# Kernel optimization log

Hardware: AMD Instinct MI355X
Metric: run time of the kernel (lower is better)

## Reference

```python
import jax, jax.numpy as jnp
import numpy as np

IN_F = 128
OUT_F = 128
GROUPS = 8
NUM_F = 8
B = 16
NP_ = 4096


def setup_inputs() -> dict:
    key = jax.random.key(0)
    ks = jax.random.split(key, 6)
    x = jax.random.normal(ks[0], (B, NP_, IN_F), dtype=jnp.float32)
    grid = jnp.arange(NUM_F, dtype=jnp.float32) + 1.0                      # [num_f]
    base_weight = jax.random.normal(ks[1], (OUT_F, IN_F), dtype=jnp.float32) * 0.05
    scale_sp = jnp.ones((OUT_F,), dtype=jnp.float32)
    coef = jax.random.uniform(ks[2], (GROUPS, 1, NUM_F), dtype=jnp.float32)
    conv_w = jax.random.normal(ks[3], (NUM_F, OUT_F, IN_F), dtype=jnp.float32) * 0.05  # grouped 1x1 conv
    conv_b = jax.random.normal(ks[4], (NUM_F, OUT_F), dtype=jnp.float32) * 0.05
    return {"x": x, "grid": grid, "base_weight": base_weight,
            "scale_sp": scale_sp, "coef": coef, "conv_w": conv_w, "conv_b": conv_b}


def reference(x, grid, base_weight, scale_sp, coef, conv_w, conv_b):
    Bd, Nd, D = x.shape
    num_f = grid.shape[0]
    groups = coef.shape[0]
    gsz = D // groups
    xf = x.reshape(Bd * Nd, D)                                  # [batch, in]
    # base path: SiLU then linear (no bias)
    base = jax.nn.silu(xf) @ base_weight.T                       # [batch, out]
    # spline path: sin(grid * x), broadcast coef per (group, f)
    s = jnp.sin(grid[None, :, None] * xf[:, None, :])            # [batch, num_f, in]
    cm = coef[:, 0, :].T                                         # [num_f, groups]
    s = s.reshape(-1, num_f, groups, gsz) * cm[None, :, :, None]
    s = s.reshape(-1, num_f, D)                                  # [batch, num_f, in]
    # grouped 1x1 conv == per-f GEMM
    spline = jnp.einsum('bfi,foi->bfo', s, conv_w) + conv_b[None]
    spline = spline.sum(axis=1) * scale_sp                       # [batch, out]
    out = (base + spline).reshape(Bd, Nd, -1)
    return out
```

## Files before the change

### kernel.cpp

```cpp
#include <hip/hip_runtime.h>
#include <hip/hip_bf16.h>
#include <stdint.h>

#define IN_F   128
#define OUT_F  128
#define NUM_F  8
#define NROWS  (16*4096)

typedef __bf16  bf16x8  __attribute__((ext_vector_type(8)));
typedef float   f32x16  __attribute__((ext_vector_type(16)));

#define LDS_HALF  (9*8*2*64*16)
#define WP_CHUNKS (2*9*8*2*64)
#define WP_BYTES  (WP_CHUNKS*16)
#define BIAS_OFF  WP_BYTES

__global__ __launch_bounds__(256) void skan_prep(
    const float* __restrict__ base_w,
    const float* __restrict__ scale,
    const float* __restrict__ coef,
    const float* __restrict__ conv_w,
    const float* __restrict__ conv_b,
    __bf16* __restrict__ Wp, float* __restrict__ bias)
{
    int gid = blockIdx.x * 256 + threadIdx.x;
    int flat = gid;
    int l  = flat & 63;  flat >>= 6;
    int t2 = flat & 1;   flat >>= 1;
    int s  = flat & 7;   flat >>= 3;
    int fb = flat % 9;
    int h2 = flat / 9;
    int n  = h2 * 64 + t2 * 32 + (l & 31);
    int k0 = s * 16 + (l >> 5) * 8;
    __bf16* dst = Wp + (size_t)gid * 8;
    if (fb == 0) {
        const float4* b4 = (const float4*)(base_w + n * IN_F + k0);
        float4 a = b4[0], b = b4[1];
        dst[0]=(__bf16)a.x; dst[1]=(__bf16)a.y; dst[2]=(__bf16)a.z; dst[3]=(__bf16)a.w;
        dst[4]=(__bf16)b.x; dst[5]=(__bf16)b.y; dst[6]=(__bf16)b.z; dst[7]=(__bf16)b.w;
    } else {
        int f = fb - 1;
        float sc = scale[n];
        const float4* c4 = (const float4*)(conv_w + ((size_t)f * OUT_F + n) * IN_F + k0);
        float4 a = c4[0], b = c4[1];
        float m0c = coef[((k0    ) >> 4) * NUM_F + f] * sc;
        float m1c = coef[((k0 + 4) >> 4) * NUM_F + f] * sc;
        (void)m1c;
        dst[0]=(__bf16)(a.x*m0c); dst[1]=(__bf16)(a.y*m0c); dst[2]=(__bf16)(a.z*m0c); dst[3]=(__bf16)(a.w*m0c);
        dst[4]=(__bf16)(b.x*m0c); dst[5]=(__bf16)(b.y*m0c); dst[6]=(__bf16)(b.z*m0c); dst[7]=(__bf16)(b.w*m0c);
    }
    if (gid < OUT_F) {
        float b = 0.f;
        #pragma unroll
        for (int f = 0; f < NUM_F; ++f) b += conv_b[f * OUT_F + gid];
        bias[gid] = b * scale[gid];
    }
}

__device__ __forceinline__ void gld_lds16(const void* g, void* l) {
    __builtin_amdgcn_global_load_lds(
        (const __attribute__((address_space(1))) uint32_t*)g,
        (__attribute__((address_space(3))) uint32_t*)l, 16, 0, 0);
}

__device__ __forceinline__ uint32_t pkbf(float a, float b) {
    __bf16 x = (__bf16)a, y = (__bf16)b;
    uint16_t ux, uy;
    __builtin_memcpy(&ux, &x, 2);
    __builtin_memcpy(&uy, &y, 2);
    return (uint32_t)ux | ((uint32_t)uy << 16);
}
__device__ __forceinline__ float upk_lo(uint32_t p) { return __uint_as_float(p << 16); }
__device__ __forceinline__ float upk_hi(uint32_t p) { return __uint_as_float(p & 0xffff0000u); }

__global__ __launch_bounds__(256, 1) void skan_main(
    const float* __restrict__ x,
    const __bf16* __restrict__ Wp,
    const float* __restrict__ bias,
    float* __restrict__ out)
{
    __shared__ __align__(16) char sB[LDS_HALF];

    const int tid  = threadIdx.x;
    const int w    = tid >> 6;
    const int l    = tid & 63;
    const int hl   = l & 31;
    const int h    = l >> 5;
    const int bx   = blockIdx.x;
    const int half = bx & 1;
    const int m0   = (bx >> 1) * 256 + w * 64;

    const char* src = (const char*)Wp + (size_t)half * LDS_HALF;
    #pragma unroll
    for (int i = 0; i < 36; ++i) {
        int off = (i * 256 + tid) * 16;
        gld_lds16(src + off, sB + off);
    }

    const float4* x4 = (const float4*)x;
    uint32_t xe[2][32];
    #pragma unroll
    for (int g = 0; g < 2; ++g) {
        size_t base = (size_t)(m0 + 32 * g + hl) * 32 + 2 * h;
        #pragma unroll
        for (int s = 0; s < 8; ++s) {
            float4 a = x4[base + 4 * s];
            float4 b = x4[base + 4 * s + 1];
            xe[g][4*s+0] = pkbf(a.x, a.y);
            xe[g][4*s+1] = pkbf(a.z, a.w);
            xe[g][4*s+2] = pkbf(b.x, b.y);
            xe[g][4*s+3] = pkbf(b.z, b.w);
        }
    }

    f32x16 acc[2][2];
    #pragma unroll
    for (int g = 0; g < 2; ++g)
        #pragma unroll
        for (int t = 0; t < 2; ++t)
            #pragma unroll
            for (int r = 0; r < 16; ++r) acc[g][t][r] = 0.f;

    __syncthreads();

    const bf16x8* bp = (const bf16x8*)sB;

    #pragma unroll
    for (int s = 0; s < 8; ++s) {
        bf16x8 a0, a1;
        #pragma unroll
        for (int g = 0; g < 2; ++g) {
            #pragma unroll
            for (int jp = 0; jp < 4; ++jp) {
                uint32_t p = xe[g][4*s+jp];
                float lo = upk_lo(p), hi = upk_hi(p);
                float slo = lo * __builtin_amdgcn_rcpf(1.0f + __expf(-lo));
                float shi = hi * __builtin_amdgcn_rcpf(1.0f + __expf(-hi));
                if (g == 0) { a0[2*jp] = (__bf16)slo; a0[2*jp+1] = (__bf16)shi; }
                else        { a1[2*jp] = (__bf16)slo; a1[2*jp+1] = (__bf16)shi; }
            }
        }
        #pragma unroll
        for (int t = 0; t < 2; ++t) {
            bf16x8 b = bp[(s * 2 + t) * 64 + l];
            acc[0][t] = __builtin_amdgcn_mfma_f32_32x32x16_bf16(a0, b, acc[0][t], 0, 0, 0);
            acc[1][t] = __builtin_amdgcn_mfma_f32_32x32x16_bf16(a1, b, acc[1][t], 0, 0, 0);
        }
    }

    #pragma unroll
    for (int s = 0; s < 8; ++s) {
        float sp[16], sp2[16], tc[16];
        #pragma unroll
        for (int g = 0; g < 2; ++g) {
            #pragma unroll
            for (int jp = 0; jp < 4; ++jp) {
                uint32_t p = xe[g][4*s+jp];
                float lo = upk_lo(p), hi = upk_hi(p);
                float rl = __builtin_amdgcn_fractf(lo * 0.15915494309189535f);
                float rh = __builtin_amdgcn_fractf(hi * 0.15915494309189535f);
                int j0 = g * 8 + 2 * jp;
                sp[j0]     = __builtin_amdgcn_sinf(rl);
                sp[j0+1]   = __builtin_amdgcn_sinf(rh);
                tc[j0]     = 2.0f * __builtin_amdgcn_cosf(rl);
                tc[j0+1]   = 2.0f * __builtin_amdgcn_cosf(rh);
                sp2[j0]    = 0.0f;
                sp2[j0+1]  = 0.0f;
            }
        }
        #pragma unroll
        for (int f = 1; f <= 8; ++f) {
            bf16x8 a0, a1;
            #pragma unroll
            for (int j = 0; j < 8; ++j) {
                a0[j] = (__bf16)sp[j];
                a1[j] = (__bf16)sp[8 + j];
            }
            #pragma unroll
            for (int t = 0; t < 2; ++t) {
                bf16x8 b = bp[((f * 8 + s) * 2 + t) * 64 + l];
                acc[0][t] = __builtin_amdgcn_mfma_f32_32x32x16_bf16(a0, b, acc[0][t], 0, 0, 0);
                acc[1][t] = __builtin_amdgcn_mfma_f32_32x32x16_bf16(a1, b, acc[1][t], 0, 0, 0);
            }
            if (f < 8) {
                #pragma unroll
                for (int i = 0; i < 16; ++i) {
                    float sn = __builtin_fmaf(tc[i], sp[i], -sp2[i]);
                    sp2[i] = sp[i];
                    sp[i]  = sn;
                }
            }
        }
    }

    #pragma unroll
    for (int g = 0; g < 2; ++g) {
        #pragma unroll
        for (int t = 0; t < 2; ++t) {
            float bv = bias[half * 64 + t * 32 + hl];
            #pragma unroll
            for (int r = 0; r < 16; ++r) {
                int row = (r & 3) + 8 * (r >> 2) + 4 * h + 32 * g;
                out[(size_t)(m0 + row) * OUT_F + half * 64 + t * 32 + hl] = acc[g][t][r] + bv;
            }
        }
    }
}

extern "C" void kernel_launch(void* const* d_in, const int* in_sizes, int n_in,
                              void* d_out, int out_size, void* d_ws, size_t ws_size,
                              hipStream_t stream) {
    const float* x      = (const float*)d_in[0];
    const float* base_w = (const float*)d_in[2];
    const float* scale  = (const float*)d_in[3];
    const float* coef   = (const float*)d_in[4];
    const float* conv_w = (const float*)d_in[5];
    const float* conv_b = (const float*)d_in[6];
    __bf16* Wp   = (__bf16*)d_ws;
    float*  bias = (float*)((char*)d_ws + BIAS_OFF);
    float*  out  = (float*)d_out;

    skan_prep<<<WP_CHUNKS / 256, 256, 0, stream>>>(base_w, scale, coef, conv_w, conv_b, Wp, bias);
    skan_main<<<(NROWS / 256) * 2, 256, 0, stream>>>(x, Wp, bias, out);
}
```

Measured before the change: 119.7 us.

## Use 1024-thread blocks with 32 rows per wave to cut LDS weight reloads

The main kernel now launches 1024-thread blocks, with each wave handling 32 rows instead of 64 (one MFMA row-group instead of two). This halves the accumulator and x registers per thread and amortizes each block's 147 KB LDS weight load over 512 rows instead of 256. It also fuses the SiLU and sine passes into one loop over k-steps. In exchange, each B fragment read from LDS now feeds only one MFMA instead of two, and there are fewer independent MFMA chains to hide latency.

```diff
diff --git a/kernel.cpp b/kernel.cpp
--- a/kernel.cpp
+++ b/kernel.cpp
@@ -43,11 +43,9 @@
         float sc = scale[n];
         const float4* c4 = (const float4*)(conv_w + ((size_t)f * OUT_F + n) * IN_F + k0);
         float4 a = c4[0], b = c4[1];
-        float m0c = coef[((k0    ) >> 4) * NUM_F + f] * sc;
-        float m1c = coef[((k0 + 4) >> 4) * NUM_F + f] * sc;
-        (void)m1c;
-        dst[0]=(__bf16)(a.x*m0c); dst[1]=(__bf16)(a.y*m0c); dst[2]=(__bf16)(a.z*m0c); dst[3]=(__bf16)(a.w*m0c);
-        dst[4]=(__bf16)(b.x*m0c); dst[5]=(__bf16)(b.y*m0c); dst[6]=(__bf16)(b.z*m0c); dst[7]=(__bf16)(b.w*m0c);
+        float mc = coef[(k0 >> 4) * NUM_F + f] * sc;
+        dst[0]=(__bf16)(a.x*mc); dst[1]=(__bf16)(a.y*mc); dst[2]=(__bf16)(a.z*mc); dst[3]=(__bf16)(a.w*mc);
+        dst[4]=(__bf16)(b.x*mc); dst[5]=(__bf16)(b.y*mc); dst[6]=(__bf16)(b.z*mc); dst[7]=(__bf16)(b.w*mc);
     }
     if (gid < OUT_F) {
         float b = 0.f;
@@ -73,7 +71,7 @@
 __device__ __forceinline__ float upk_lo(uint32_t p) { return __uint_as_float(p << 16); }
 __device__ __forceinline__ float upk_hi(uint32_t p) { return __uint_as_float(p & 0xffff0000u); }
 
-__global__ __launch_bounds__(256, 1) void skan_main(
+__global__ __launch_bounds__(1024, 4) void skan_main(
     const float* __restrict__ x,
     const __bf16* __restrict__ Wp,
     const float* __restrict__ bias,
@@ -88,38 +86,35 @@
     const int h    = l >> 5;
     const int bx   = blockIdx.x;
     const int half = bx & 1;
-    const int m0   = (bx >> 1) * 256 + w * 64;
+    const int m0   = (bx >> 1) * 512 + w * 32;
 
     const char* src = (const char*)Wp + (size_t)half * LDS_HALF;
     #pragma unroll
-    for (int i = 0; i < 36; ++i) {
-        int off = (i * 256 + tid) * 16;
+    for (int i = 0; i < 9; ++i) {
+        int off = (i * 1024 + tid) * 16;
         gld_lds16(src + off, sB + off);
     }
 
     const float4* x4 = (const float4*)x;
-    uint32_t xe[2][32];
-    #pragma unroll
-    for (int g = 0; g < 2; ++g) {
-        size_t base = (size_t)(m0 + 32 * g + hl) * 32 + 2 * h;
+    uint32_t xe[32];
+    {
+        size_t base = (size_t)(m0 + hl) * 32 + 2 * h;
         #pragma unroll
         for (int s = 0; s < 8; ++s) {
             float4 a = x4[base + 4 * s];
             float4 b = x4[base + 4 * s + 1];
-            xe[g][4*s+0] = pkbf(a.x, a.y);
-            xe[g][4*s+1] = pkbf(a.z, a.w);
-            xe[g][4*s+2] = pkbf(b.x, b.y);
-            xe[g][4*s+3] = pkbf(b.z, b.w);
-        }
-    }
-
-    f32x16 acc[2][2];
-    #pragma unroll
-    for (int g = 0; g < 2; ++g)
-        #pragma unroll
-        for (int t = 0; t < 2; ++t)
-            #pragma unroll
-            for (int r = 0; r < 16; ++r) acc[g][t][r] = 0.f;
+            xe[4*s+0] = pkbf(a.x, a.y);
+            xe[4*s+1] = pkbf(a.z, a.w);
+            xe[4*s+2] = pkbf(b.x, b.y);
+            xe[4*s+3] = pkbf(b.z, b.w);
+        }
+    }
+
+    f32x16 acc[2];
+    #pragma unroll
+    for (int t = 0; t < 2; ++t)
+        #pragma unroll
+        for (int r = 0; r < 16; ++r) acc[t][r] = 0.f;
 
     __syncthreads();
 
@@ -127,64 +122,48 @@
 
     #pragma unroll
     for (int s = 0; s < 8; ++s) {
-        bf16x8 a0, a1;
-        #pragma unroll
-        for (int g = 0; g < 2; ++g) {
+        {
+            bf16x8 a;
             #pragma unroll
             for (int jp = 0; jp < 4; ++jp) {
-                uint32_t p = xe[g][4*s+jp];
+                uint32_t p = xe[4*s+jp];
                 float lo = upk_lo(p), hi = upk_hi(p);
-                float slo = lo * __builtin_amdgcn_rcpf(1.0f + __expf(-lo));
-                float shi = hi * __builtin_amdgcn_rcpf(1.0f + __expf(-hi));
-                if (g == 0) { a0[2*jp] = (__bf16)slo; a0[2*jp+1] = (__bf16)shi; }
-                else        { a1[2*jp] = (__bf16)slo; a1[2*jp+1] = (__bf16)shi; }
-            }
-        }
-        #pragma unroll
-        for (int t = 0; t < 2; ++t) {
-            bf16x8 b = bp[(s * 2 + t) * 64 + l];
-            acc[0][t] = __builtin_amdgcn_mfma_f32_32x32x16_bf16(a0, b, acc[0][t], 0, 0, 0);
-            acc[1][t] = __builtin_amdgcn_mfma_f32_32x32x16_bf16(a1, b, acc[1][t], 0, 0, 0);
-        }
-    }
-
-    #pragma unroll
-    for (int s = 0; s < 8; ++s) {
-        float sp[16], sp2[16], tc[16];
-        #pragma unroll
-        for (int g = 0; g < 2; ++g) {
-            #pragma unroll
-            for (int jp = 0; jp < 4; ++jp) {
-                uint32_t p = xe[g][4*s+jp];
-                float lo = upk_lo(p), hi = upk_hi(p);
-                float rl = __builtin_amdgcn_fractf(lo * 0.15915494309189535f);
-                float rh = __builtin_amdgcn_fractf(hi * 0.15915494309189535f);
-                int j0 = g * 8 + 2 * jp;
-                sp[j0]     = __builtin_amdgcn_sinf(rl);
-                sp[j0+1]   = __builtin_amdgcn_sinf(rh);
-                tc[j0]     = 2.0f * __builtin_amdgcn_cosf(rl);
-                tc[j0+1]   = 2.0f * __builtin_amdgcn_cosf(rh);
-                sp2[j0]    = 0.0f;
-                sp2[j0+1]  = 0.0f;
-            }
+                a[2*jp]   = (__bf16)(lo * __builtin_amdgcn_rcpf(1.0f + __expf(-lo)));
+                a[2*jp+1] = (__bf16)(hi * __builtin_amdgcn_rcpf(1.0f + __expf(-hi)));
+            }
+            #pragma unroll
+            for (int t = 0; t < 2; ++t) {
+                bf16x8 b = bp[(s * 2 + t) * 64 + l];
+                acc[t] = __builtin_amdgcn_mfma_f32_32x32x16_bf16(a, b, acc[t], 0, 0, 0);
+            }
+        }
+        float sp[8], sp2[8], tc[8];
+        #pragma unroll
+        for (int jp = 0; jp < 4; ++jp) {
+            uint32_t p = xe[4*s+jp];
+            float lo = upk_lo(p), hi = upk_hi(p);
+            float rl = __builtin_amdgcn_fractf(lo * 0.15915494309189535f);
+            float rh = __builtin_amdgcn_fractf(hi * 0.15915494309189535f);
+            sp[2*jp]    = __builtin_amdgcn_sinf(rl);
+            sp[2*jp+1]  = __builtin_amdgcn_sinf(rh);
+            tc[2*jp]    = 2.0f * __builtin_amdgcn_cosf(rl);
+            tc[2*jp+1]  = 2.0f * __builtin_amdgcn_cosf(rh);
+            sp2[2*jp]   = 0.0f;
+            sp2[2*jp+1] = 0.0f;
         }
         #pragma unroll
         for (int f = 1; f <= 8; ++f) {
-            bf16x8 a0, a1;
-            #pragma unroll
-            for (int j = 0; j < 8; ++j) {
-                a0[j] = (__bf16)sp[j];
-                a1[j] = (__bf16)sp[8 + j];
-            }
+            bf16x8 a;
+            #pragma unroll
+            for (int j = 0; j < 8; ++j) a[j] = (__bf16)sp[j];
             #pragma unroll
             for (int t = 0; t < 2; ++t) {
                 bf16x8 b = bp[((f * 8 + s) * 2 + t) * 64 + l];
-                acc[0][t] = __builtin_amdgcn_mfma_f32_32x32x16_bf16(a0, b, acc[0][t], 0, 0, 0);
-                acc[1][t] = __builtin_amdgcn_mfma_f32_32x32x16_bf16(a1, b, acc[1][t], 0, 0, 0);
+                acc[t] = __builtin_amdgcn_mfma_f32_32x32x16_bf16(a, b, acc[t], 0, 0, 0);
             }
             if (f < 8) {
                 #pragma unroll
-                for (int i = 0; i < 16; ++i) {
+                for (int i = 0; i < 8; ++i) {
                     float sn = __builtin_fmaf(tc[i], sp[i], -sp2[i]);
                     sp2[i] = sp[i];
                     sp[i]  = sn;
@@ -194,15 +173,12 @@
     }
 
     #pragma unroll
-    for (int g = 0; g < 2; ++g) {
-        #pragma unroll
-        for (int t = 0; t < 2; ++t) {
-            float bv = bias[half * 64 + t * 32 + hl];
-            #pragma unroll
-            for (int r = 0; r < 16; ++r) {
-                int row = (r & 3) + 8 * (r >> 2) + 4 * h + 32 * g;
-                out[(size_t)(m0 + row) * OUT_F + half * 64 + t * 32 + hl] = acc[g][t][r] + bv;
-            }
+    for (int t = 0; t < 2; ++t) {
+        float bv = bias[half * 64 + t * 32 + hl];
+        #pragma unroll
+        for (int r = 0; r < 16; ++r) {
+            int row = (r & 3) + 8 * (r >> 2) + 4 * h;
+            out[(size_t)(m0 + row) * OUT_F + half * 64 + t * 32 + hl] = acc[t][r] + bv;
         }
     }
 }
@@ -221,5 +197,5 @@
     float*  out  = (float*)d_out;
 
     skan_prep<<<WP_CHUNKS / 256, 256, 0, stream>>>(base_w, scale, coef, conv_w, conv_b, Wp, bias);
-    skan_main<<<(NROWS / 256) * 2, 256, 0, stream>>>(x, Wp, bias, out);
-}
+    skan_main<<<(NROWS / 512) * 2, 1024, 0, stream>>>(x, Wp, bias, out);
+}
```

Measured after the change: 117.3 us. 2.0% less time.

## Use 512-thread blocks with one wave of 256 blocks and packed bf16 fragments

Applied to the files above, without the earlier changes.

The main kernel now runs 512-thread blocks (8 waves, 512 rows each), and the grid shrinks to 256 blocks ordered half-major. Each block loads the 147 KB weight half into LDS once and amortizes that load over twice as many rows, with far fewer blocks in total. The SiLU GEMM loop is fused into the per-s spline loop, and A fragments are built by packing bf16 pairs into 32-bit words instead of inserting single elements. The risk is higher register pressure under launch_bounds(512,2). Each CU can hold only one block because of LDS size, so one block per CU may expose the load latency.

```diff
diff --git a/kernel.cpp b/kernel.cpp
--- a/kernel.cpp
+++ b/kernel.cpp
@@ -43,11 +43,9 @@
         float sc = scale[n];
         const float4* c4 = (const float4*)(conv_w + ((size_t)f * OUT_F + n) * IN_F + k0);
         float4 a = c4[0], b = c4[1];
-        float m0c = coef[((k0    ) >> 4) * NUM_F + f] * sc;
-        float m1c = coef[((k0 + 4) >> 4) * NUM_F + f] * sc;
-        (void)m1c;
-        dst[0]=(__bf16)(a.x*m0c); dst[1]=(__bf16)(a.y*m0c); dst[2]=(__bf16)(a.z*m0c); dst[3]=(__bf16)(a.w*m0c);
-        dst[4]=(__bf16)(b.x*m0c); dst[5]=(__bf16)(b.y*m0c); dst[6]=(__bf16)(b.z*m0c); dst[7]=(__bf16)(b.w*m0c);
+        float mc = coef[(k0 >> 4) * NUM_F + f] * sc;
+        dst[0]=(__bf16)(a.x*mc); dst[1]=(__bf16)(a.y*mc); dst[2]=(__bf16)(a.z*mc); dst[3]=(__bf16)(a.w*mc);
+        dst[4]=(__bf16)(b.x*mc); dst[5]=(__bf16)(b.y*mc); dst[6]=(__bf16)(b.z*mc); dst[7]=(__bf16)(b.w*mc);
     }
     if (gid < OUT_F) {
         float b = 0.f;
@@ -73,7 +71,14 @@
 __device__ __forceinline__ float upk_lo(uint32_t p) { return __uint_as_float(p << 16); }
 __device__ __forceinline__ float upk_hi(uint32_t p) { return __uint_as_float(p & 0xffff0000u); }
 
-__global__ __launch_bounds__(256, 1) void skan_main(
+__device__ __forceinline__ bf16x8 mkfrag(uint32_t p0, uint32_t p1, uint32_t p2, uint32_t p3) {
+    uint32_t u[4] = {p0, p1, p2, p3};
+    bf16x8 r;
+    __builtin_memcpy(&r, u, 16);
+    return r;
+}
+
+__global__ __launch_bounds__(512, 2) void skan_main(
     const float* __restrict__ x,
     const __bf16* __restrict__ Wp,
     const float* __restrict__ bias,
@@ -87,13 +92,14 @@
     const int hl   = l & 31;
     const int h    = l >> 5;
     const int bx   = blockIdx.x;
-    const int half = bx & 1;
-    const int m0   = (bx >> 1) * 256 + w * 64;
+    const int rowb = bx & 127;
+    const int half = bx >> 7;
+    const int m0   = rowb * 512 + w * 64;
 
     const char* src = (const char*)Wp + (size_t)half * LDS_HALF;
     #pragma unroll
-    for (int i = 0; i < 36; ++i) {
-        int off = (i * 256 + tid) * 16;
+    for (int i = 0; i < 18; ++i) {
+        int off = (i * 512 + tid) * 16;
         gld_lds16(src + off, sB + off);
     }
 
@@ -127,32 +133,31 @@
 
     #pragma unroll
     for (int s = 0; s < 8; ++s) {
-        bf16x8 a0, a1;
-        #pragma unroll
-        for (int g = 0; g < 2; ++g) {
-            #pragma unroll
-            for (int jp = 0; jp < 4; ++jp) {
-                uint32_t p = xe[g][4*s+jp];
-                float lo = upk_lo(p), hi = upk_hi(p);
-                float slo = lo * __builtin_amdgcn_rcpf(1.0f + __expf(-lo));
-                float shi = hi * __builtin_amdgcn_rcpf(1.0f + __expf(-hi));
-                if (g == 0) { a0[2*jp] = (__bf16)slo; a0[2*jp+1] = (__bf16)shi; }
-                else        { a1[2*jp] = (__bf16)slo; a1[2*jp+1] = (__bf16)shi; }
-            }
-        }
-        #pragma unroll
-        for (int t = 0; t < 2; ++t) {
-            bf16x8 b = bp[(s * 2 + t) * 64 + l];
-            acc[0][t] = __builtin_amdgcn_mfma_f32_32x32x16_bf16(a0, b, acc[0][t], 0, 0, 0);
-            acc[1][t] = __builtin_amdgcn_mfma_f32_32x32x16_bf16(a1, b, acc[1][t], 0, 0, 0);
-        }
-    }
-
-    #pragma unroll
-    for (int s = 0; s < 8; ++s) {
+        {
+            bf16x8 af[2];
+            #pragma unroll
+            for (int g = 0; g < 2; ++g) {
+                uint32_t pr[4];
+                #pragma unroll
+                for (int jp = 0; jp < 4; ++jp) {
+                    uint32_t p = xe[g][4*s+jp];
+                    float lo = upk_lo(p), hi = upk_hi(p);
+                    float slo = lo * __builtin_amdgcn_rcpf(1.0f + __expf(-lo));
+                    float shi = hi * __builtin_amdgcn_rcpf(1.0f + __expf(-hi));
+                    pr[jp] = pkbf(slo, shi);
+                }
+                af[g] = mkfrag(pr[0], pr[1], pr[2], pr[3]);
+            }
+            #pragma unroll
+            for (int t = 0; t < 2; ++t) {
+                bf16x8 b = bp[(s * 2 + t) * 64 + l];
+                acc[0][t] = __builtin_amdgcn_mfma_f32_32x32x16_bf16(af[0], b, acc[0][t], 0, 0, 0);
+                acc[1][t] = __builtin_amdgcn_mfma_f32_32x32x16_bf16(af[1], b, acc[1][t], 0, 0, 0);
+            }
+        }
         float sp[16], sp2[16], tc[16];
         #pragma unroll
-        for (int g = 0; g < 2; ++g) {
+        for (int g = 0; g < 2; ++g)
             #pragma unroll
             for (int jp = 0; jp < 4; ++jp) {
                 uint32_t p = xe[g][4*s+jp];
@@ -160,22 +165,19 @@
                 float rl = __builtin_amdgcn_fractf(lo * 0.15915494309189535f);
                 float rh = __builtin_amdgcn_fractf(hi * 0.15915494309189535f);
                 int j0 = g * 8 + 2 * jp;
-                sp[j0]     = __builtin_amdgcn_sinf(rl);
-                sp[j0+1]   = __builtin_amdgcn_sinf(rh);
-                tc[j0]     = 2.0f * __builtin_amdgcn_cosf(rl);
-                tc[j0+1]   = 2.0f * __builtin_amdgcn_cosf(rh);
-                sp2[j0]    = 0.0f;
-                sp2[j0+1]  = 0.0f;
-            }
-        }
+                sp[j0]    = __builtin_amdgcn_sinf(rl);
+                sp[j0+1]  = __builtin_amdgcn_sinf(rh);
+                tc[j0]    = 2.0f * __builtin_amdgcn_cosf(rl);
+                tc[j0+1]  = 2.0f * __builtin_amdgcn_cosf(rh);
+                sp2[j0]   = 0.0f;
+                sp2[j0+1] = 0.0f;
+            }
         #pragma unroll
         for (int f = 1; f <= 8; ++f) {
-            bf16x8 a0, a1;
-            #pragma unroll
-            for (int j = 0; j < 8; ++j) {
-                a0[j] = (__bf16)sp[j];
-                a1[j] = (__bf16)sp[8 + j];
-            }
+            bf16x8 a0 = mkfrag(pkbf(sp[0], sp[1]),  pkbf(sp[2], sp[3]),
+                               pkbf(sp[4], sp[5]),  pkbf(sp[6], sp[7]));
+            bf16x8 a1 = mkfrag(pkbf(sp[8], sp[9]),  pkbf(sp[10], sp[11]),
+                               pkbf(sp[12], sp[13]), pkbf(sp[14], sp[15]));
             #pragma unroll
             for (int t = 0; t < 2; ++t) {
                 bf16x8 b = bp[((f * 8 + s) * 2 + t) * 64 + l];
@@ -194,7 +196,7 @@
     }
 
     #pragma unroll
-    for (int g = 0; g < 2; ++g) {
+    for (int g = 0; g < 2; ++g)
         #pragma unroll
         for (int t = 0; t < 2; ++t) {
             float bv = bias[half * 64 + t * 32 + hl];
@@ -204,7 +206,6 @@
                 out[(size_t)(m0 + row) * OUT_F + half * 64 + t * 32 + hl] = acc[g][t][r] + bv;
             }
         }
-    }
 }
 
 extern "C" void kernel_launch(void* const* d_in, const int* in_sizes, int n_in,
@@ -221,5 +222,5 @@
     float*  out  = (float*)d_out;
 
     skan_prep<<<WP_CHUNKS / 256, 256, 0, stream>>>(base_w, scale, coef, conv_w, conv_b, Wp, bias);
-    skan_main<<<(NROWS / 256) * 2, 256, 0, stream>>>(x, Wp, bias, out);
-}
+    skan_main<<<256, 512, 0, stream>>>(x, Wp, bias, out);
+}
```

Measured after the change: 125.0 us. 4.4% more time.
